# Kernel optimization log

Hardware: AMD Instinct MI355X
Metric: run time of the kernel (lower is better)

The kernel has to match this reference:

```python
import jax, jax.numpy as jnp
import numpy as np

BATCH = 16384
IN_F = 1024
OUT_F = 1024
NUM_BASIS = 8
DEGREE = 3
K = NUM_BASIS + DEGREE  # 11 basis columns
EPS = 1e-5


def _knots():
    return jnp.linspace(0.0, 1.0, K + 1)


def _compute_basis(x):
    """Cox-de Boor recursion, faithful to the torch in-place variant:
    at degree d only columns j < K-d are updated; higher columns keep
    their lower-degree values (and are still contracted in the einsum).
    x: [B, IN_F] -> basis: [B, IN_F, K]
    """
    knots = _knots().astype(x.dtype)
    xa = x[..., None]  # [B, IN_F, 1]
    # degree-0 indicator: x in [knots[j], knots[j+1])
    basis = ((xa >= knots[:K]) & (xa < knots[1:K + 1])).astype(x.dtype)
    for d in range(1, DEGREE + 1):
        m = K - d
        denom1 = knots[d:K] - knots[:m]            # [m]
        denom2 = knots[d + 1:K + 1] - knots[1:m + 1]  # [m]
        safe1 = jnp.where(denom1 != 0, denom1, 1.0)
        safe2 = jnp.where(denom2 != 0, denom2, 1.0)
        alpha = jnp.where(denom1 != 0, (xa - knots[:m]) / safe1, 0.0)
        beta = jnp.where(denom2 != 0, (knots[d + 1:K + 1] - xa) / safe2, 0.0)
        new = alpha * basis[..., :m] + beta * basis[..., 1:m + 1]
        basis = jnp.concatenate([new, basis[..., m:]], axis=-1)
    return basis


def setup_inputs() -> dict:
    key = jax.random.key(0)
    k1, k2, k3, k4 = jax.random.split(key, 4)
    x = jax.random.uniform(k1, (BATCH, IN_F), dtype=jnp.float32)
    # Xavier-uniform control points [out, in, K]
    bound_cp = float(np.sqrt(6.0 / (IN_F + K)))  # torch xavier treats last dims as fan
    control_points = jax.random.uniform(k2, (OUT_F, IN_F, K), minval=-bound_cp, maxval=bound_cp, dtype=jnp.float32)
    bound_w = float(np.sqrt(6.0 / (IN_F + OUT_F)))
    W = jax.random.uniform(k3, (OUT_F, IN_F), minval=-bound_w, maxval=bound_w, dtype=jnp.float32)
    b = jnp.zeros((OUT_F,), dtype=jnp.float32)
    gamma = jnp.ones((OUT_F,), dtype=jnp.float32)
    beta = jnp.zeros((OUT_F,), dtype=jnp.float32)
    return {"x": x, "control_points": control_points, "W": W, "b": b,
            "gamma": gamma, "beta": beta}


def reference(x, control_points, W, b, gamma, beta):
    basis = _compute_basis(x)  # [B, IN_F, K]
    spline_out = jnp.einsum('bik,oik->bo', basis, control_points)  # [B, OUT_F]
    out = spline_out + x @ W.T + b
    # LayerNorm over last dim (dropout is identity in eval / p used as 0)
    mu = jnp.mean(out, axis=-1, keepdims=True)
    var = jnp.mean(jnp.square(out - mu), axis=-1, keepdims=True)
    return gamma * (out - mu) * jax.lax.rsqrt(var + EPS) + beta
```

## Files before the change

### kernel.cpp

```cpp
#include <hip/hip_runtime.h>
#include <hip/hip_bf16.h>

#define BATCH   16384
#define IN_F    1024
#define OUT_F   1024
#define KCOLS   11
#define KPL     12
#define KP      (KPL*IN_F)
#define KHALF   (KP/2)
#define NTKH    (KHALF/64)
#define NITH    (NTKH/2)
#define LN_EPS  1e-5f

typedef __attribute__((ext_vector_type(8))) short short8;
typedef __attribute__((ext_vector_type(4))) float f32x4;

static __device__ __forceinline__ unsigned short f2bf(float f) {
  __hip_bfloat16 h = __float2bfloat16(f);
  return *reinterpret_cast<unsigned short*>(&h);
}

__device__ __forceinline__ void bspline_basis(float x, float bas[KCOLS]) {
  const float s = 1.0f / 11.0f;
  float kn[12];
#pragma unroll
  for (int j = 0; j < 12; ++j) kn[j] = (float)j * s;
  kn[11] = 1.0f;
#pragma unroll
  for (int j = 0; j < 11; ++j)
    bas[j] = (x >= kn[j] && x < kn[j + 1]) ? 1.0f : 0.0f;
#pragma unroll
  for (int d = 1; d <= 3; ++d) {
#pragma unroll
    for (int j = 0; j < 11 - d; ++j) {
      const float r1 = 1.0f / (kn[j + d] - kn[j]);
      const float r2 = 1.0f / (kn[j + d + 1] - kn[j + 1]);
      float a = (x - kn[j]) * r1;
      float c = (kn[j + d + 1] - x) * r2;
      bas[j] = a * bas[j] + c * bas[j + 1];
    }
  }
}

__global__ __launch_bounds__(256) void featgen(const float* __restrict__ X,
                                               unsigned short* __restrict__ A,
                                               int row0) {
  const int brow = blockIdx.x;
  const int i0 = threadIdx.x * 4;
  const float4 xv = *reinterpret_cast<const float4*>(X + (size_t)(row0 + brow) * IN_F + i0);
  float xs[4] = {xv.x, xv.y, xv.z, xv.w};
  float bas[4][KCOLS];
#pragma unroll
  for (int t = 0; t < 4; ++t) bspline_basis(xs[t], bas[t]);
  unsigned short* outp = A + (size_t)brow * KP + i0;
#pragma unroll
  for (int k = 0; k < KCOLS; ++k) {
    ushort4 u;
    u.x = f2bf(bas[0][k]); u.y = f2bf(bas[1][k]);
    u.z = f2bf(bas[2][k]); u.w = f2bf(bas[3][k]);
    *reinterpret_cast<ushort4*>(outp + (size_t)k * IN_F) = u;
  }
  ushort4 u;
  u.x = f2bf(xs[0]); u.y = f2bf(xs[1]); u.z = f2bf(xs[2]); u.w = f2bf(xs[3]);
  *reinterpret_cast<ushort4*>(outp + (size_t)KCOLS * IN_F) = u;
}

__global__ __launch_bounds__(256) void bgen(const float* __restrict__ CP,
                                            const float* __restrict__ W,
                                            unsigned short* __restrict__ Bm) {
  const int o = blockIdx.x;
  const int i0 = threadIdx.x * 4;
  unsigned short* outp = Bm + (size_t)o * KP + i0;
#pragma unroll
  for (int k = 0; k < KCOLS; ++k) {
    ushort4 u;
    u.x = f2bf(CP[((size_t)o * IN_F + i0 + 0) * KCOLS + k]);
    u.y = f2bf(CP[((size_t)o * IN_F + i0 + 1) * KCOLS + k]);
    u.z = f2bf(CP[((size_t)o * IN_F + i0 + 2) * KCOLS + k]);
    u.w = f2bf(CP[((size_t)o * IN_F + i0 + 3) * KCOLS + k]);
    *reinterpret_cast<ushort4*>(outp + (size_t)k * IN_F) = u;
  }
  ushort4 u;
  u.x = f2bf(W[(size_t)o * IN_F + i0 + 0]);
  u.y = f2bf(W[(size_t)o * IN_F + i0 + 1]);
  u.z = f2bf(W[(size_t)o * IN_F + i0 + 2]);
  u.w = f2bf(W[(size_t)o * IN_F + i0 + 3]);
  *reinterpret_cast<ushort4*>(outp + (size_t)KCOLS * IN_F) = u;
}


#define BAR()    __builtin_amdgcn_s_barrier()
#define SCHED0() __builtin_amdgcn_sched_barrier(0)
#define WAITV(N) asm volatile("s_waitcnt vmcnt(" #N ")" ::: "memory")

__global__ __launch_bounds__(512, 2) void gemm8p(const unsigned short* __restrict__ A,
                                                 const unsigned short* __restrict__ Bm,
                                                 float* __restrict__ Cc,
                                                 float* __restrict__ Cp, int nbm) {
  __shared__ unsigned short lds[2][2][2][128 * 64];
  const int tid  = (int)threadIdx.x;
  const int lane = tid & 63;
  const int w    = tid >> 6;
  const int wm   = w >> 2;
  const int wn   = w & 3;

  const int nwg = nbm * 8;
  const int cpx = nwg >> 3;
  const int bid = (int)blockIdx.x;
  const int swz = (bid & 7) * cpx + (bid >> 3);
  const int bn = swz & 3;
  const int ks = (swz >> 2) & 1;
  const int bm = swz >> 3;
  const size_t koff = (size_t)ks * KHALF;
  float* __restrict__ C = ks ? Cp : Cc;

  const int srow = (w << 3) + (lane >> 3);
  const int scol = ((lane & 7) ^ (lane >> 3)) << 3;
  const unsigned short* aB = A  + (size_t)(bm * 256 + srow) * KP + koff + scol;
  const unsigned short* bB = Bm + (size_t)(bn * 256 + srow) * KP + koff + scol;

#define STAGE(T, AB, H, BUF)                                                          \
  do {                                                                                \
    if ((T) < NTKH) {                                                                 \
      const unsigned short* g_ = ((AB) ? bB : aB) + (size_t)(H) * 128 * KP + (size_t)(T) * 64; \
      unsigned short* l_ = &lds[BUF][AB][H][w * 512];                                 \
      __builtin_amdgcn_global_load_lds((const __attribute__((address_space(1))) void*)g_,       \
                                       (__attribute__((address_space(3))) void*)l_, 16, 0, 0);  \
      __builtin_amdgcn_global_load_lds((const __attribute__((address_space(1))) void*)(g_ + (size_t)64 * KP), \
                                       (__attribute__((address_space(3))) void*)(l_ + 4096), 16, 0, 0); \
    }                                                                                 \
  } while (0)

  const int fr = lane & 15;
  const int g4 = lane >> 4;
  const int s7 = lane & 7;
  const int col0 = ((g4 ^ s7) << 3);
  const int col1 = (((4 + g4) ^ s7) << 3);
  const unsigned short* aH[2] = {&lds[0][0][wm][0], &lds[1][0][wm][0]};
  const unsigned short* bH[2] = {&lds[0][1][wn >> 1][0], &lds[1][1][wn >> 1][0]};
  const int brow0 = (wn & 1) * 64;

  short8 aF[4][2], bF[4][2];
  f32x4 acc[8][4] = {};

#define LOADA(MB, BUF)                                                         \
  do {                                                                         \
    _Pragma("unroll") for (int m_ = 0; m_ < 4; ++m_) {                         \
      const unsigned short* p_ = aH[BUF] + ((MB) + m_) * 1024 + fr * 64;       \
      aF[m_][0] = *reinterpret_cast<const short8*>(p_ + col0);                 \
      aF[m_][1] = *reinterpret_cast<const short8*>(p_ + col1);                 \
    }                                                                          \
  } while (0)

#define LOADB4(BUF)                                                            \
  do {                                                                         \
    _Pragma("unroll") for (int n_ = 0; n_ < 4; ++n_) {                         \
      const unsigned short* p_ = bH[BUF] + (brow0 + n_ * 16 + fr) * 64;        \
      bF[n_][0] = *reinterpret_cast<const short8*>(p_ + col0);                 \
      bF[n_][1] = *reinterpret_cast<const short8*>(p_ + col1);                 \
    }                                                                          \
  } while (0)

#define MFMAH(MB)                                                              \
  do {                                                                         \
    __builtin_amdgcn_s_setprio(1);                                             \
    _Pragma("unroll") for (int m_ = 0; m_ < 4; ++m_)                           \
    _Pragma("unroll") for (int n_ = 0; n_ < 4; ++n_)                           \
    _Pragma("unroll") for (int kk_ = 0; kk_ < 2; ++kk_)                        \
      acc[(MB) + m_][n_] = __builtin_amdgcn_mfma_f32_16x16x32_bf16(            \
          aF[m_][kk_], bF[n_][kk_], acc[(MB) + m_][n_], 0, 0, 0);              \
    __builtin_amdgcn_s_setprio(0);                                             \
  } while (0)

  STAGE(0, 0, 0, 0); STAGE(0, 0, 1, 0);
  STAGE(0, 1, 0, 0); STAGE(0, 1, 1, 0);
  STAGE(1, 1, 0, 1); STAGE(1, 1, 1, 1);
  WAITV(4);
  BAR();

#pragma unroll 1
  for (int j = 0; j < NITH; ++j) {
    const int tb = 2 * j + 1, t2 = 2 * j + 2, t3 = 2 * j + 3;
    LOADA(0, 0); LOADB4(0);
    STAGE(tb, 0, 0, 1); STAGE(tb, 0, 1, 1);
    MFMAH(0);
    SCHED0(); BAR();
    LOADA(4, 0);
    STAGE(t2, 1, 0, 0); STAGE(t2, 1, 1, 0);
    MFMAH(4);
    if (j < NITH - 1) { WAITV(4); } else { WAITV(0); }
    SCHED0(); BAR();
    LOADA(0, 1); LOADB4(1);
    STAGE(t2, 0, 0, 0); STAGE(t2, 0, 1, 0);
    MFMAH(0);
    SCHED0(); BAR();
    LOADA(4, 1);
    STAGE(t3, 1, 0, 1); STAGE(t3, 1, 1, 1);
    MFMAH(4);
    if (j < NITH - 1) { WAITV(4); } else { WAITV(0); }
    SCHED0(); BAR();
  }

  const size_t r0 = (size_t)bm * 256 + wm * 128 + (lane >> 4) * 4;
  const int c0 = bn * 256 + wn * 64 + fr;
#pragma unroll
  for (int m = 0; m < 8; ++m)
#pragma unroll
    for (int n = 0; n < 4; ++n)
#pragma unroll
      for (int r = 0; r < 4; ++r)
        C[(r0 + m * 16 + r) * OUT_F + (c0 + n * 16)] = acc[m][n][r];
}

__global__ __launch_bounds__(256) void ln_kernel(float* __restrict__ C,
                                                 const float* __restrict__ P,
                                                 const float* __restrict__ bias,
                                                 const float* __restrict__ gamma,
                                                 const float* __restrict__ beta) {
  const int row = blockIdx.x;
  const int tid = threadIdx.x;
  float4 v = *reinterpret_cast<const float4*>(C + (size_t)row * OUT_F + tid * 4);
  const float4 p = *reinterpret_cast<const float4*>(P + (size_t)row * OUT_F + tid * 4);
  const float4 bb = *reinterpret_cast<const float4*>(bias + tid * 4);
  v.x += p.x + bb.x; v.y += p.y + bb.y; v.z += p.z + bb.z; v.w += p.w + bb.w;
  float s = v.x + v.y + v.z + v.w;
  float q = v.x * v.x + v.y * v.y + v.z * v.z + v.w * v.w;
#pragma unroll
  for (int off = 32; off > 0; off >>= 1) {
    s += __shfl_down(s, off);
    q += __shfl_down(q, off);
  }
  __shared__ float red[8];
  const int wave = tid >> 6, lane = tid & 63;
  if (lane == 0) { red[wave] = s; red[4 + wave] = q; }
  __syncthreads();
  s = red[0] + red[1] + red[2] + red[3];
  q = red[4] + red[5] + red[6] + red[7];
  const float mu = s * (1.0f / OUT_F);
  const float var = q * (1.0f / OUT_F) - mu * mu;
  const float rs = rsqrtf(var + LN_EPS);
  const float4 g = *reinterpret_cast<const float4*>(gamma + tid * 4);
  const float4 be = *reinterpret_cast<const float4*>(beta + tid * 4);
  float4 o;
  o.x = g.x * (v.x - mu) * rs + be.x;
  o.y = g.y * (v.y - mu) * rs + be.y;
  o.z = g.z * (v.z - mu) * rs + be.z;
  o.w = g.w * (v.w - mu) * rs + be.w;
  *reinterpret_cast<float4*>(C + (size_t)row * OUT_F + tid * 4) = o;
}

extern "C" void kernel_launch(void* const* d_in, const int* in_sizes, int n_in,
                              void* d_out, int out_size, void* d_ws, size_t ws_size,
                              hipStream_t stream) {
  const float* x     = (const float*)d_in[0];
  const float* cp    = (const float*)d_in[1];
  const float* W     = (const float*)d_in[2];
  const float* bias  = (const float*)d_in[3];
  const float* gamma = (const float*)d_in[4];
  const float* beta  = (const float*)d_in[5];
  float* out = (float*)d_out;

  unsigned short* Bm = (unsigned short*)d_ws;
  const size_t bBytes = (size_t)OUT_F * KP * sizeof(unsigned short);
  size_t avail = ws_size > bBytes ? ws_size - bBytes : 0;
  const size_t perRow = (size_t)KP * 2 + (size_t)OUT_F * 4;
  long long fit = (long long)(avail / perRow);
  int chunk;
  if (fit >= BATCH)     chunk = BATCH;
  else if (fit >= 8192) chunk = 8192;
  else                  chunk = (int)((fit / 256) * 256);
  if (chunk < 256) chunk = 256;

  unsigned short* Af = (unsigned short*)((char*)d_ws + bBytes);
  float* P = (float*)(Af + (size_t)chunk * KP);

  bgen<<<OUT_F, 256, 0, stream>>>(cp, W, Bm);
  for (int r0 = 0; r0 < BATCH; r0 += chunk) {
    const int rows = (BATCH - r0 < chunk) ? (BATCH - r0) : chunk;
    featgen<<<rows, 256, 0, stream>>>(x, Af, r0);
    const int nbm = rows / 256;
    gemm8p<<<nbm * 8, 512, 0, stream>>>(Af, Bm, out + (size_t)r0 * OUT_F, P, nbm);
    ln_kernel<<<rows, 256, 0, stream>>>(out + (size_t)r0 * OUT_F, P, bias, gamma, beta);
  }
}
```

Baseline: 448.3 us.

## Retile GEMM to 256x128 tiles, K=32 steps, triple-buffered LDS at higher occupancy

Replaces the 256x256 tile GEMM with a 256x128 tile, a 32-wide K step and a three-stage LDS ring buffer. Launch bounds go up to 4 blocks per SM and the grid doubles to 16 workgroups per M block. The aim is to raise occupancy and shrink the per-block LDS and register footprint, so latency is hidden through more concurrent waves and deeper prefetch. The trade-off is lower arithmetic intensity per tile, since A is re-read twice as often, plus more barriers per unit of K work.

```diff
diff --git a/kernel.cpp b/kernel.cpp
--- a/kernel.cpp
+++ b/kernel.cpp
@@ -8,8 +8,7 @@
 #define KPL     12
 #define KP      (KPL*IN_F)
 #define KHALF   (KP/2)
-#define NTKH    (KHALF/64)
-#define NITH    (NTKH/2)
+#define NT      (KHALF/32)
 #define LN_EPS  1e-5f
 
 typedef __attribute__((ext_vector_type(8))) short short8;
@@ -93,120 +92,116 @@
 #define SCHED0() __builtin_amdgcn_sched_barrier(0)
 #define WAITV(N) asm volatile("s_waitcnt vmcnt(" #N ")" ::: "memory")
 
-__global__ __launch_bounds__(512, 2) void gemm8p(const unsigned short* __restrict__ A,
-                                                 const unsigned short* __restrict__ Bm,
-                                                 float* __restrict__ Cc,
-                                                 float* __restrict__ Cp, int nbm) {
-  __shared__ unsigned short lds[2][2][2][128 * 64];
+__global__ __launch_bounds__(512, 4) void gemmk(const unsigned short* __restrict__ A,
+                                                const unsigned short* __restrict__ Bm,
+                                                float* __restrict__ Cc,
+                                                float* __restrict__ Cp, int nbm) {
+  __shared__ unsigned short ldsA[3][256 * 32];
+  __shared__ unsigned short ldsB[3][128 * 32];
   const int tid  = (int)threadIdx.x;
   const int lane = tid & 63;
   const int w    = tid >> 6;
   const int wm   = w >> 2;
   const int wn   = w & 3;
 
-  const int nwg = nbm * 8;
+  const int nwg = nbm * 16;
   const int cpx = nwg >> 3;
   const int bid = (int)blockIdx.x;
   const int swz = (bid & 7) * cpx + (bid >> 3);
-  const int bn = swz & 3;
-  const int ks = (swz >> 2) & 1;
-  const int bm = swz >> 3;
+  const int bn = swz & 7;
+  const int ks = (swz >> 3) & 1;
+  const int bm = swz >> 4;
   const size_t koff = (size_t)ks * KHALF;
   float* __restrict__ C = ks ? Cp : Cc;
 
-  const int srow = (w << 3) + (lane >> 3);
-  const int scol = ((lane & 7) ^ (lane >> 3)) << 3;
-  const unsigned short* aB = A  + (size_t)(bm * 256 + srow) * KP + koff + scol;
-  const unsigned short* bB = Bm + (size_t)(bn * 256 + srow) * KP + koff + scol;
-
-#define STAGE(T, AB, H, BUF)                                                          \
+  const int srow = tid >> 2;
+  const int schunk = (tid & 3) ^ ((tid >> 3) & 3);
+  const unsigned short* aSrc = A  + (size_t)(bm * 256 + srow) * KP + koff + schunk * 8;
+  const unsigned short* bSrc = Bm + (size_t)(bn * 128 + srow) * KP + koff + schunk * 8;
+
+#define STAGE_A(T, ISS, BUF)                                                          \
   do {                                                                                \
-    if ((T) < NTKH) {                                                                 \
-      const unsigned short* g_ = ((AB) ? bB : aB) + (size_t)(H) * 128 * KP + (size_t)(T) * 64; \
-      unsigned short* l_ = &lds[BUF][AB][H][w * 512];                                 \
-      __builtin_amdgcn_global_load_lds((const __attribute__((address_space(1))) void*)g_,       \
-                                       (__attribute__((address_space(3))) void*)l_, 16, 0, 0);  \
-      __builtin_amdgcn_global_load_lds((const __attribute__((address_space(1))) void*)(g_ + (size_t)64 * KP), \
-                                       (__attribute__((address_space(3))) void*)(l_ + 4096), 16, 0, 0); \
+    if ((T) < NT) {                                                                   \
+      const unsigned short* g_ = aSrc + (size_t)(ISS) * 128 * KP + (size_t)(T) * 32;  \
+      __builtin_amdgcn_global_load_lds((const __attribute__((address_space(1))) void*)g_, \
+          (__attribute__((address_space(3))) void*)(&ldsA[BUF][(ISS) * 4096 + w * 512]), 16, 0, 0); \
+    }                                                                                 \
+  } while (0)
+
+#define STAGE_B(T, BUF)                                                               \
+  do {                                                                               \
+    if ((T) < NT) {                                                                   \
+      const unsigned short* g_ = bSrc + (size_t)(T) * 32;                             \
+      __builtin_amdgcn_global_load_lds((const __attribute__((address_space(1))) void*)g_, \
+          (__attribute__((address_space(3))) void*)(&ldsB[BUF][w * 512]), 16, 0, 0);  \
     }                                                                                 \
   } while (0)
 
   const int fr = lane & 15;
   const int g4 = lane >> 4;
-  const int s7 = lane & 7;
-  const int col0 = ((g4 ^ s7) << 3);
-  const int col1 = (((4 + g4) ^ s7) << 3);
-  const unsigned short* aH[2] = {&lds[0][0][wm][0], &lds[1][0][wm][0]};
-  const unsigned short* bH[2] = {&lds[0][1][wn >> 1][0], &lds[1][1][wn >> 1][0]};
-  const int brow0 = (wn & 1) * 64;
-
-  short8 aF[4][2], bF[4][2];
-  f32x4 acc[8][4] = {};
-
-#define LOADA(MB, BUF)                                                         \
-  do {                                                                         \
-    _Pragma("unroll") for (int m_ = 0; m_ < 4; ++m_) {                         \
-      const unsigned short* p_ = aH[BUF] + ((MB) + m_) * 1024 + fr * 64;       \
-      aF[m_][0] = *reinterpret_cast<const short8*>(p_ + col0);                 \
-      aF[m_][1] = *reinterpret_cast<const short8*>(p_ + col1);                 \
-    }                                                                          \
-  } while (0)
-
-#define LOADB4(BUF)                                                            \
-  do {                                                                         \
-    _Pragma("unroll") for (int n_ = 0; n_ < 4; ++n_) {                         \
-      const unsigned short* p_ = bH[BUF] + (brow0 + n_ * 16 + fr) * 64;        \
-      bF[n_][0] = *reinterpret_cast<const short8*>(p_ + col0);                 \
-      bF[n_][1] = *reinterpret_cast<const short8*>(p_ + col1);                 \
-    }                                                                          \
+  const int colx = ((g4 ^ ((fr >> 1) & 3)) << 3);
+
+  short8 aF[4], bF[2];
+  f32x4 acc[8][2] = {};
+
+#define LOADA4(MB, BUF)                                                        \
+  do {                                                                         \
+    _Pragma("unroll") for (int m_ = 0; m_ < 4; ++m_)                           \
+      aF[m_] = *reinterpret_cast<const short8*>(                               \
+          &ldsA[BUF][(wm * 128 + ((MB) + m_) * 16 + fr) * 32 + colx]);         \
+  } while (0)
+
+#define LOADB2(BUF)                                                            \
+  do {                                                                         \
+    _Pragma("unroll") for (int n_ = 0; n_ < 2; ++n_)                           \
+      bF[n_] = *reinterpret_cast<const short8*>(                               \
+          &ldsB[BUF][(wn * 32 + n_ * 16 + fr) * 32 + colx]);                   \
   } while (0)
 
 #define MFMAH(MB)                                                              \
   do {                                                                         \
     __builtin_amdgcn_s_setprio(1);                                             \
     _Pragma("unroll") for (int m_ = 0; m_ < 4; ++m_)                           \
-    _Pragma("unroll") for (int n_ = 0; n_ < 4; ++n_)                           \
-    _Pragma("unroll") for (int kk_ = 0; kk_ < 2; ++kk_)                        \
+    _Pragma("unroll") for (int n_ = 0; n_ < 2; ++n_)                           \
       acc[(MB) + m_][n_] = __builtin_amdgcn_mfma_f32_16x16x32_bf16(            \
-          aF[m_][kk_], bF[n_][kk_], acc[(MB) + m_][n_], 0, 0, 0);              \
+          aF[m_], bF[n_], acc[(MB) + m_][n_], 0, 0, 0);                        \
     __builtin_amdgcn_s_setprio(0);                                             \
   } while (0)
 
-  STAGE(0, 0, 0, 0); STAGE(0, 0, 1, 0);
-  STAGE(0, 1, 0, 0); STAGE(0, 1, 1, 0);
-  STAGE(1, 1, 0, 1); STAGE(1, 1, 1, 1);
-  WAITV(4);
+#define ITER(T, CUR, NX2)                                                      \
+  do {                                                                         \
+                                           \
+    LOADB2(CUR); LOADA4(0, CUR);                                               \
+    STAGE_A((T) + 2, 0, NX2); STAGE_A((T) + 2, 1, NX2);                        \
+    MFMAH(0);                                                                  \
+    SCHED0(); BAR();                                                           \
+                    \
+    LOADA4(4, CUR);                                                            \
+    STAGE_B((T) + 2, NX2);                                                     \
+    MFMAH(4);                                                                  \
+    if ((T) < NT - 2) { WAITV(3); } else { WAITV(0); }                         \
+    SCHED0(); BAR();                                                           \
+  } while (0)
+
+  STAGE_A(0, 0, 0); STAGE_A(0, 1, 0); STAGE_B(0, 0);
+  STAGE_A(1, 0, 1); STAGE_A(1, 1, 1); STAGE_B(1, 1);
+  WAITV(3);
   BAR();
 
 #pragma unroll 1
-  for (int j = 0; j < NITH; ++j) {
-    const int tb = 2 * j + 1, t2 = 2 * j + 2, t3 = 2 * j + 3;
-    LOADA(0, 0); LOADB4(0);
-    STAGE(tb, 0, 0, 1); STAGE(tb, 0, 1, 1);
-    MFMAH(0);
-    SCHED0(); BAR();
-    LOADA(4, 0);
-    STAGE(t2, 1, 0, 0); STAGE(t2, 1, 1, 0);
-    MFMAH(4);
-    if (j < NITH - 1) { WAITV(4); } else { WAITV(0); }
-    SCHED0(); BAR();
-    LOADA(0, 1); LOADB4(1);
-    STAGE(t2, 0, 0, 0); STAGE(t2, 0, 1, 0);
-    MFMAH(0);
-    SCHED0(); BAR();
-    LOADA(4, 1);
-    STAGE(t3, 1, 0, 1); STAGE(t3, 1, 1, 1);
-    MFMAH(4);
-    if (j < NITH - 1) { WAITV(4); } else { WAITV(0); }
-    SCHED0(); BAR();
+  for (int jg = 0; jg < NT / 3; ++jg) {
+    const int t0 = jg * 3;
+    ITER(t0 + 0, 0, 2);
+    ITER(t0 + 1, 1, 0);
+    ITER(t0 + 2, 2, 1);
   }
 
   const size_t r0 = (size_t)bm * 256 + wm * 128 + (lane >> 4) * 4;
-  const int c0 = bn * 256 + wn * 64 + fr;
+  const int c0 = bn * 128 + wn * 32 + fr;
 #pragma unroll
   for (int m = 0; m < 8; ++m)
 #pragma unroll
-    for (int n = 0; n < 4; ++n)
+    for (int n = 0; n < 2; ++n)
 #pragma unroll
       for (int r = 0; r < 4; ++r)
         C[(r0 + m * 16 + r) * OUT_F + (c0 + n * 16)] = acc[m][n][r];
@@ -279,7 +274,7 @@
     const int rows = (BATCH - r0 < chunk) ? (BATCH - r0) : chunk;
     featgen<<<rows, 256, 0, stream>>>(x, Af, r0);
     const int nbm = rows / 256;
-    gemm8p<<<nbm * 8, 512, 0, stream>>>(Af, Bm, out + (size_t)r0 * OUT_F, P, nbm);
+    gemmk<<<nbm * 16, 512, 0, stream>>>(Af, Bm, out + (size_t)r0 * OUT_F, P, nbm);
     ln_kernel<<<rows, 256, 0, stream>>>(out + (size_t)r0 * OUT_F, P, bias, gamma, beta);
   }
 }
```

After: 590.7 us. 1.32x slower.
